# Kernel tuning notes

Hardware: AMD Instinct MI355X
Metric: run time of the kernel (lower is better)

The kernel has to match this reference:

```python
import jax, jax.numpy as jnp
import numpy as np

N = 50000
E = 800000
F_IN, F_HID, F_OUT = 128, 128, 64


def setup_inputs() -> dict:
    key = jax.random.key(0)
    ks = jax.random.split(key, 8)
    x = jax.random.normal(ks[0], (N, F_IN), dtype=jnp.float32)
    attn_edge_index = jax.random.randint(ks[1], (2, E), 0, N, dtype=jnp.int64)
    attn_edge_weight = jax.random.uniform(ks[2], (E,), dtype=jnp.float32)
    # GCNConv params (glorot-ish scale); PyG lin has no bias, conv bias added after aggregation
    W1 = jax.random.normal(ks[3], (F_IN, F_HID), dtype=jnp.float32) * (1.0 / np.sqrt(F_IN))
    b1 = jnp.zeros((F_HID,), dtype=jnp.float32)
    W2 = jax.random.normal(ks[4], (F_HID, F_OUT), dtype=jnp.float32) * (1.0 / np.sqrt(F_HID))
    b2 = jnp.zeros((F_OUT,), dtype=jnp.float32)
    return {"x": x, "attn_edge_index": attn_edge_index, "attn_edge_weight": attn_edge_weight,
            "W1": W1, "b1": b1, "W2": W2, "b2": b2}


def _gcn_norm(edge_index, edge_weight, num_nodes):
    # Add self-loops with weight 1 (PyG gcn_norm default)
    loop = jnp.arange(num_nodes, dtype=edge_index.dtype)
    src = jnp.concatenate([edge_index[0], loop])
    dst = jnp.concatenate([edge_index[1], loop])
    w = jnp.concatenate([edge_weight, jnp.ones((num_nodes,), edge_weight.dtype)])
    deg = jax.ops.segment_sum(w, dst, num_segments=num_nodes)  # in-degree weighted
    dinv = jnp.where(deg > 0, jax.lax.rsqrt(deg), 0.0)
    norm = dinv[src] * w * dinv[dst]  # symmetric normalization
    return src, dst, norm


def _gcn_conv(h, src, dst, norm, W, b, num_nodes):
    h = h @ W                                   # [N, Fout] dense transform
    msg = norm[:, None] * h[src]                # [E+N, Fout] gather-multiply
    out = jax.ops.segment_sum(msg, dst, num_segments=num_nodes)  # scatter-add
    return out + b


def reference(x, attn_edge_index, attn_edge_weight, W1, b1, W2, b2):
    num_nodes = x.shape[0]
    src, dst, norm = _gcn_norm(attn_edge_index, attn_edge_weight, num_nodes)
    h = _gcn_conv(x, src, dst, norm, W1, b1, num_nodes)
    h = jax.nn.relu(h)
    # dropout(p=0.5) is identity in eval mode
    h = _gcn_conv(h, src, dst, norm, W2, b2, num_nodes)
    return h
```

## Files before the change

kernel.cpp:

```cpp
#include <hip/hip_runtime.h>
#include <hip/hip_bf16.h>

static constexpr int FIN   = 128;
static constexpr int FHID  = 128;
static constexpr int FOUTC = 64;
static constexpr int CAP   = 64;

typedef short bf16x8 __attribute__((ext_vector_type(8)));
typedef float f32x4 __attribute__((ext_vector_type(4)));
typedef unsigned u32x2 __attribute__((ext_vector_type(2)));
typedef unsigned u32x4 __attribute__((ext_vector_type(4)));

__device__ __forceinline__ float bfbits2f(unsigned short u) {
  union { unsigned i; float f; } c; c.i = ((unsigned)u) << 16; return c.f;
}
__device__ __forceinline__ float wbits2f(unsigned u) {
  union { unsigned i; float f; } c; c.i = u; return c.f;
}
__device__ __forceinline__ unsigned f2wbits(float f) {
  union { float fv; unsigned i; } c; c.fv = f; return c.i;
}
__device__ __forceinline__ void unpack_bf2(unsigned u, float& lo, float& hi) {
  union { unsigned i; float f; } a, b;
  a.i = u << 16;
  b.i = u & 0xffff0000u;
  lo = a.f; hi = b.f;
}
__device__ __forceinline__ unsigned short f2bfbits(float f) {
  union { float fv; unsigned i; } c; c.fv = f;
  unsigned i = c.i;
  unsigned r = i + 0x7FFFu + ((i >> 16) & 1u);
  if ((i & 0x7F800000u) == 0x7F800000u) r = i;
  return (unsigned short)(r >> 16);
}
__device__ __forceinline__ int ld_idx(const void* ei, int is64, long long off) {
  return is64 ? (int)((const long long*)ei)[off] : ((const int*)ei)[off];
}
__device__ __forceinline__ float ld_f(const void* p, int isbf, long long i) {
  return isbf ? bfbits2f(((const unsigned short*)p)[i]) : ((const float*)p)[i];
}

__global__ void setup_kernel(const unsigned short* __restrict__ xb,
                             const unsigned* __restrict__ eiw,
                             const void* __restrict__ W1, const void* __restrict__ W2,
                             int* __restrict__ flags, unsigned short* __restrict__ Wt1,
                             unsigned short* __restrict__ Wt2, uint4* __restrict__ ellz,
                             int nell4) {
  const int tid = threadIdx.x;
  const int gid = blockIdx.x * 256 + tid;
  __shared__ int sflags[2];
  if (tid < 64) {
    unsigned short xs = xb[2 * tid];
    unsigned long long mb = __ballot(((xs >> 7) & 0xFFu) >= 0xC0u);
    unsigned long long m2 = __ballot(eiw[2 * tid + 1] != 0u);
    if (tid == 0) {
      sflags[0] = (mb == 0ull);
      sflags[1] = (m2 == 0ull);
      if (blockIdx.x == 0) { flags[0] = sflags[0]; flags[1] = sflags[1]; }
    }
  }
  __syncthreads();
  int f = sflags[0];
  if (blockIdx.x < 96) {
    int i = gid;
    if (i < 128 * 128) {
      int k = i >> 7, nn = i & 127;
      Wt1[nn * 128 + k] = f2bfbits(ld_f(W1, f, i));
    } else {
      int j = i - 128 * 128;
      int k = j >> 6, nn = j & 63;
      Wt2[nn * 128 + k] = f2bfbits(ld_f(W2, f, j));
    }
  }
  uint4 z = make_uint4(0u, 0u, 0u, 0u);
  for (int j = gid; j < nell4; j += gridDim.x * 256) ellz[j] = z;
}

__global__ void fill_ell(const void* __restrict__ ei, const void* __restrict__ ew,
                         const int* __restrict__ flg, unsigned long long* __restrict__ ell,
                         int E, int half) {
  int g = blockIdx.x * 256 + threadIdx.x;
  if (g >= half) return;
  int is64 = flg[1], isbf = flg[0];
  int sA = ld_idx(ei, is64, g);
  int dA = ld_idx(ei, is64, (long long)E + g);
  unsigned wA = f2wbits(ld_f(ew, isbf, g));
  int eB = g + half;
  bool hasB = eB < E;
  int sB = 0, dB = 0;
  unsigned wB = 0u;
  if (hasB) {
    sB = ld_idx(ei, is64, eB);
    dB = ld_idx(ei, is64, (long long)E + eB);
    wB = f2wbits(ld_f(ew, isbf, eB));
  }
  unsigned long long vA = ((unsigned long long)wA << 32) | (unsigned)sA;
  unsigned long long vB = ((unsigned long long)wB << 32) | (unsigned)sB;
  unsigned long long* rowA = ell + (size_t)dA * CAP;
  unsigned long long* rowB = ell + (size_t)dB * CAP;
  int pA = g & (CAP - 1), pB = eB & (CAP - 1);
  bool doneA = (vA == 0ull);
  bool doneB = !hasB || (vB == 0ull);
  unsigned long long oA = doneA ? 0ull : atomicCAS(&rowA[pA], 0ull, vA);
  unsigned long long oB = doneB ? 0ull : atomicCAS(&rowB[pB], 0ull, vB);
  for (int t = 1; t < CAP && !doneA && oA != 0ull; ++t) {
    pA = (pA + 1) & (CAP - 1);
    oA = atomicCAS(&rowA[pA], 0ull, vA);
  }
  for (int t = 1; t < CAP && !doneB && oB != 0ull; ++t) {
    pB = (pB + 1) & (CAP - 1);
    oB = atomicCAS(&rowB[pB], 0ull, vB);
  }
}

__global__ void dinv_compact(uint2* __restrict__ ell, float* __restrict__ dinv,
                             unsigned* __restrict__ cedge, int n) {
  int wid = (blockIdx.x * 256 + threadIdx.x) >> 6;
  int lane = threadIdx.x & 63;
  if (wid >= n) return;
  u32x2 rv = __builtin_nontemporal_load((const u32x2*)(ell + (size_t)wid * CAP) + lane);
  float w = wbits2f(rv.y);
  float ws = w;
#pragma unroll
  for (int off = 1; off < 64; off <<= 1) ws += __shfl_xor(ws, off);
  bool valid = rv.y != 0u;
  unsigned long long m = __ballot(valid);
  int c = __popcll(m);
  int rank = __popcll(m & ((1ull << lane) - 1ull));
  int destl = valid ? rank : c + (lane - rank);
  unsigned entry = valid ? ((rv.x << 16) | (unsigned)f2bfbits(w)) : 0u;
  int pe = __builtin_amdgcn_ds_permute(destl << 2, (int)entry);
  cedge[(size_t)wid * (CAP * 2) + lane] = (unsigned)pe;
  if (lane == 0) dinv[wid] = rsqrtf(1.f + ws);
}

__launch_bounds__(256)
__global__ void gather_l1(const void* __restrict__ x, const int* __restrict__ flg,
                          const unsigned* __restrict__ cedge, const float* __restrict__ dinv,
                          unsigned* __restrict__ agg, int n) {
  int wid = (blockIdx.x * 256 + threadIdx.x) >> 6;
  int lane = threadIdx.x & 63;
  if (wid >= n) return;
  unsigned e = __builtin_nontemporal_load(cedge + (size_t)wid * (CAP * 2) + lane);
  unsigned long long m = __ballot(e != 0u);
  int c = __popcll(m);
  int rsrc = (int)(e >> 16);
  float rw = (lane < c) ? bfbits2f((unsigned short)(e & 0xFFFFu)) * dinv[rsrc] : 0.f;
  float di = dinv[wid];

  if (flg[0]) {
    const uint4* xv = (const uint4*)x;
    const int fgrp = lane & 15, egrp = lane >> 4;
    float acc[8];
#pragma unroll
    for (int k = 0; k < 8; ++k) acc[k] = 0.f;
    int iters = (c + 15) >> 4;
    for (int it = 0; it < iters; ++it) {
      int b = it * 16 + egrp;
      int i0 = b, i1 = b + 4, i2 = b + 8, i3 = b + 12;
      int s0 = __shfl(rsrc, i0), s1 = __shfl(rsrc, i1);
      int s2 = __shfl(rsrc, i2), s3 = __shfl(rsrc, i3);
      float w0 = __shfl(rw, i0), w1 = __shfl(rw, i1);
      float w2 = __shfl(rw, i2), w3 = __shfl(rw, i3);
      s0 = i0 < c ? s0 : wid;
      s1 = i1 < c ? s1 : wid;
      s2 = i2 < c ? s2 : wid;
      s3 = i3 < c ? s3 : wid;
      uint4 u0 = xv[(size_t)s0 * 16 + fgrp];
      uint4 u1 = xv[(size_t)s1 * 16 + fgrp];
      uint4 u2 = xv[(size_t)s2 * 16 + fgrp];
      uint4 u3 = xv[(size_t)s3 * 16 + fgrp];
      float l, h;
      unpack_bf2(u0.x, l, h); acc[0] = fmaf(w0, l, acc[0]); acc[1] = fmaf(w0, h, acc[1]);
      unpack_bf2(u0.y, l, h); acc[2] = fmaf(w0, l, acc[2]); acc[3] = fmaf(w0, h, acc[3]);
      unpack_bf2(u0.z, l, h); acc[4] = fmaf(w0, l, acc[4]); acc[5] = fmaf(w0, h, acc[5]);
      unpack_bf2(u0.w, l, h); acc[6] = fmaf(w0, l, acc[6]); acc[7] = fmaf(w0, h, acc[7]);
      unpack_bf2(u1.x, l, h); acc[0] = fmaf(w1, l, acc[0]); acc[1] = fmaf(w1, h, acc[1]);
      unpack_bf2(u1.y, l, h); acc[2] = fmaf(w1, l, acc[2]); acc[3] = fmaf(w1, h, acc[3]);
      unpack_bf2(u1.z, l, h); acc[4] = fmaf(w1, l, acc[4]); acc[5] = fmaf(w1, h, acc[5]);
      unpack_bf2(u1.w, l, h); acc[6] = fmaf(w1, l, acc[6]); acc[7] = fmaf(w1, h, acc[7]);
      unpack_bf2(u2.x, l, h); acc[0] = fmaf(w2, l, acc[0]); acc[1] = fmaf(w2, h, acc[1]);
      unpack_bf2(u2.y, l, h); acc[2] = fmaf(w2, l, acc[2]); acc[3] = fmaf(w2, h, acc[3]);
      unpack_bf2(u2.z, l, h); acc[4] = fmaf(w2, l, acc[4]); acc[5] = fmaf(w2, h, acc[5]);
      unpack_bf2(u2.w, l, h); acc[6] = fmaf(w2, l, acc[6]); acc[7] = fmaf(w2, h, acc[7]);
      unpack_bf2(u3.x, l, h); acc[0] = fmaf(w3, l, acc[0]); acc[1] = fmaf(w3, h, acc[1]);
      unpack_bf2(u3.y, l, h); acc[2] = fmaf(w3, l, acc[2]); acc[3] = fmaf(w3, h, acc[3]);
      unpack_bf2(u3.z, l, h); acc[4] = fmaf(w3, l, acc[4]); acc[5] = fmaf(w3, h, acc[5]);
      unpack_bf2(u3.w, l, h); acc[6] = fmaf(w3, l, acc[6]); acc[7] = fmaf(w3, h, acc[7]);
    }
#pragma unroll
    for (int k = 0; k < 8; ++k) {
      acc[k] += __shfl_xor(acc[k], 16);
      acc[k] += __shfl_xor(acc[k], 32);
    }
    if (lane < 16) {
      uint4 su = xv[(size_t)wid * 16 + fgrp];
      float s0, s1, s2, s3, s4, s5, s6, s7;
      unpack_bf2(su.x, s0, s1); unpack_bf2(su.y, s2, s3);
      unpack_bf2(su.z, s4, s5); unpack_bf2(su.w, s6, s7);
      float dd = di * di;
      float o0 = di * acc[0] + dd * s0, o1 = di * acc[1] + dd * s1;
      float o2 = di * acc[2] + dd * s2, o3 = di * acc[3] + dd * s3;
      float o4 = di * acc[4] + dd * s4, o5 = di * acc[5] + dd * s5;
      float o6 = di * acc[6] + dd * s6, o7 = di * acc[7] + dd * s7;
      u32x4 pk;
      pk.x = (unsigned)f2bfbits(o0) | ((unsigned)f2bfbits(o1) << 16);
      pk.y = (unsigned)f2bfbits(o2) | ((unsigned)f2bfbits(o3) << 16);
      pk.z = (unsigned)f2bfbits(o4) | ((unsigned)f2bfbits(o5) << 16);
      pk.w = (unsigned)f2bfbits(o6) | ((unsigned)f2bfbits(o7) << 16);
      __builtin_nontemporal_store(pk, (u32x4*)agg + (size_t)wid * 16 + fgrp);
    }
  } else {
    const float4* xf = (const float4*)x;
    const int fgrp = lane & 31, egrp = lane >> 5;
    float acc[4] = {0.f, 0.f, 0.f, 0.f};
    int it8 = (c + 7) >> 3;
    for (int it = 0; it < it8; ++it) {
      int b = it * 8 + egrp;
#pragma unroll
      for (int t = 0; t < 4; ++t) {
        int idx = b + t * 2;
        int s = __shfl(rsrc, idx);
        float w = __shfl(rw, idx);
        s = idx < c ? s : wid;
        float4 v = xf[(size_t)s * 32 + fgrp];
        acc[0] = fmaf(w, v.x, acc[0]); acc[1] = fmaf(w, v.y, acc[1]);
        acc[2] = fmaf(w, v.z, acc[2]); acc[3] = fmaf(w, v.w, acc[3]);
      }
    }
#pragma unroll
    for (int k = 0; k < 4; ++k) acc[k] += __shfl_xor(acc[k], 32);
    if (lane < 32) {
      float4 sv = xf[(size_t)wid * 32 + fgrp];
      float dd = di * di;
      float o0 = di * acc[0] + dd * sv.x, o1 = di * acc[1] + dd * sv.y;
      float o2 = di * acc[2] + dd * sv.z, o3 = di * acc[3] + dd * sv.w;
      uint2 pk;
      pk.x = (unsigned)f2bfbits(o0) | ((unsigned)f2bfbits(o1) << 16);
      pk.y = (unsigned)f2bfbits(o2) | ((unsigned)f2bfbits(o3) << 16);
      ((uint2*)agg)[(size_t)wid * 32 + fgrp] = pk;
    }
  }
}

__launch_bounds__(256)
__global__ void gather_l2(const unsigned short* __restrict__ hw2, const int* __restrict__ flg,
                          const unsigned* __restrict__ cedge, const float* __restrict__ dinv,
                          const void* __restrict__ b2, void* __restrict__ out, int n) {
  int wid = (blockIdx.x * 256 + threadIdx.x) >> 6;
  int lane = threadIdx.x & 63;
  if (wid >= n) return;
  unsigned e = __builtin_nontemporal_load(cedge + (size_t)wid * (CAP * 2) + lane);
  unsigned long long m = __ballot(e != 0u);
  int c = __popcll(m);
  int rsrc = (int)(e >> 16);
  float rw = (lane < c) ? bfbits2f((unsigned short)(e & 0xFFFFu)) * dinv[rsrc] : 0.f;
  float di = dinv[wid];

  const uint4* hv = (const uint4*)hw2;
  const int fgrp = lane & 7, egrp = lane >> 3;
  float acc[8];
#pragma unroll
  for (int k = 0; k < 8; ++k) acc[k] = 0.f;
  int iters = (c + 15) >> 4;
  for (int it = 0; it < iters; ++it) {
    int i0 = it * 16 + egrp, i1 = i0 + 8;
    int s0 = __shfl(rsrc, i0), s1 = __shfl(rsrc, i1);
    float w0 = __shfl(rw, i0), w1 = __shfl(rw, i1);
    s0 = i0 < c ? s0 : wid;
    s1 = i1 < c ? s1 : wid;
    uint4 u0 = hv[(size_t)s0 * 8 + fgrp];
    uint4 u1 = hv[(size_t)s1 * 8 + fgrp];
    float l, h;
    unpack_bf2(u0.x, l, h); acc[0] = fmaf(w0, l, acc[0]); acc[1] = fmaf(w0, h, acc[1]);
    unpack_bf2(u0.y, l, h); acc[2] = fmaf(w0, l, acc[2]); acc[3] = fmaf(w0, h, acc[3]);
    unpack_bf2(u0.z, l, h); acc[4] = fmaf(w0, l, acc[4]); acc[5] = fmaf(w0, h, acc[5]);
    unpack_bf2(u0.w, l, h); acc[6] = fmaf(w0, l, acc[6]); acc[7] = fmaf(w0, h, acc[7]);
    unpack_bf2(u1.x, l, h); acc[0] = fmaf(w1, l, acc[0]); acc[1] = fmaf(w1, h, acc[1]);
    unpack_bf2(u1.y, l, h); acc[2] = fmaf(w1, l, acc[2]); acc[3] = fmaf(w1, h, acc[3]);
    unpack_bf2(u1.z, l, h); acc[4] = fmaf(w1, l, acc[4]); acc[5] = fmaf(w1, h, acc[5]);
    unpack_bf2(u1.w, l, h); acc[6] = fmaf(w1, l, acc[6]); acc[7] = fmaf(w1, h, acc[7]);
  }
#pragma unroll
  for (int k = 0; k < 8; ++k) {
    acc[k] += __shfl_xor(acc[k], 8);
    acc[k] += __shfl_xor(acc[k], 16);
    acc[k] += __shfl_xor(acc[k], 32);
  }
  if (lane < 8) {
    int isbf = flg[0];
    uint4 su = hv[(size_t)wid * 8 + fgrp];
    float s0, s1, s2, s3, s4, s5, s6, s7;
    unpack_bf2(su.x, s0, s1); unpack_bf2(su.y, s2, s3);
    unpack_bf2(su.z, s4, s5); unpack_bf2(su.w, s6, s7);
    float dd = di * di;
    float o0 = di * acc[0] + dd * s0 + ld_f(b2, isbf, fgrp * 8 + 0);
    float o1 = di * acc[1] + dd * s1 + ld_f(b2, isbf, fgrp * 8 + 1);
    float o2 = di * acc[2] + dd * s2 + ld_f(b2, isbf, fgrp * 8 + 2);
    float o3 = di * acc[3] + dd * s3 + ld_f(b2, isbf, fgrp * 8 + 3);
    float o4 = di * acc[4] + dd * s4 + ld_f(b2, isbf, fgrp * 8 + 4);
    float o5 = di * acc[5] + dd * s5 + ld_f(b2, isbf, fgrp * 8 + 5);
    float o6 = di * acc[6] + dd * s6 + ld_f(b2, isbf, fgrp * 8 + 6);
    float o7 = di * acc[7] + dd * s7 + ld_f(b2, isbf, fgrp * 8 + 7);
    if (isbf) {
      uint4 pk;
      pk.x = (unsigned)f2bfbits(o0) | ((unsigned)f2bfbits(o1) << 16);
      pk.y = (unsigned)f2bfbits(o2) | ((unsigned)f2bfbits(o3) << 16);
      pk.z = (unsigned)f2bfbits(o4) | ((unsigned)f2bfbits(o5) << 16);
      pk.w = (unsigned)f2bfbits(o6) | ((unsigned)f2bfbits(o7) << 16);
      ((uint4*)out)[(size_t)wid * 8 + fgrp] = pk;
    } else {
      ((float4*)out)[(size_t)wid * 16 + fgrp * 2 + 0] = make_float4(o0, o1, o2, o3);
      ((float4*)out)[(size_t)wid * 16 + fgrp * 2 + 1] = make_float4(o4, o5, o6, o7);
    }
  }
}

__launch_bounds__(256)
__global__ void gemm12(const unsigned short* __restrict__ agg1,
                       const unsigned short* __restrict__ Wt1,
                       const unsigned short* __restrict__ Wt2,
                       const void* __restrict__ b1, const int* __restrict__ flg,
                       unsigned short* __restrict__ hw2, int M) {
  __shared__ unsigned short As[128 * 128];
  __shared__ unsigned short W1s[128 * 128];
  __shared__ unsigned short W2s[64 * 128];
  const int tid = threadIdx.x;
  const int r0 = blockIdx.x * 128;

  for (int i = tid; i < 128 * 16; i += 256) {
    int r = i >> 4, ch = i & 15;
    uint4 v = make_uint4(0u, 0u, 0u, 0u);
    if (r0 + r < M) v = *(const uint4*)(agg1 + (size_t)(r0 + r) * 128 + ch * 8);
    *(uint4*)&As[r * 128 + ((ch ^ (r & 15)) << 3)] = v;
  }
  for (int i = tid; i < 128 * 16; i += 256) {
    int r = i >> 4, ch = i & 15;
    uint4 v = *(const uint4*)(Wt1 + (size_t)r * 128 + ch * 8);
    *(uint4*)&W1s[r * 128 + ((ch ^ (r & 15)) << 3)] = v;
  }
  for (int i = tid; i < 64 * 16; i += 256) {
    int r = i >> 4, ch = i & 15;
    uint4 v = *(const uint4*)(Wt2 + (size_t)r * 128 + ch * 8);
    *(uint4*)&W2s[r * 128 + ((ch ^ (r & 15)) << 3)] = v;
  }
  __syncthreads();

  const int lane = tid & 63;
  const int wv = tid >> 6;
  const int ln15 = lane & 15;
  const int kq = lane >> 4;
  const int wbf = flg[0];

  f32x4 acc1[2][8];
#pragma unroll
  for (int mi = 0; mi < 2; ++mi)
#pragma unroll
    for (int nt = 0; nt < 8; ++nt) acc1[mi][nt] = (f32x4){0.f, 0.f, 0.f, 0.f};
#pragma unroll
  for (int kc = 0; kc < 4; ++kc) {
    int coff = (((kc * 4 + kq) ^ ln15) << 3);
    bf16x8 a0 = *(const bf16x8*)&As[((2 * wv + 0) * 16 + ln15) * 128 + coff];
    bf16x8 a1 = *(const bf16x8*)&As[((2 * wv + 1) * 16 + ln15) * 128 + coff];
#pragma unroll
    for (int nt = 0; nt < 8; ++nt) {
      bf16x8 b = *(const bf16x8*)&W1s[(nt * 16 + ln15) * 128 + coff];
      acc1[0][nt] = __builtin_amdgcn_mfma_f32_16x16x32_bf16(a0, b, acc1[0][nt], 0, 0, 0);
      acc1[1][nt] = __builtin_amdgcn_mfma_f32_16x16x32_bf16(a1, b, acc1[1][nt], 0, 0, 0);
    }
  }

#pragma unroll
  for (int nt = 0; nt < 8; ++nt) {
    int col = nt * 16 + ln15;
    float bv = ld_f(b1, wbf, col);
#pragma unroll
    for (int mi = 0; mi < 2; ++mi) {
#pragma unroll
      for (int r = 0; r < 4; ++r) {
        int row = 32 * wv + mi * 16 + kq * 4 + r;
        float o = fmaxf(acc1[mi][nt][r] + bv, 0.f);
        As[row * 128 + ((((col >> 3)) ^ (row & 15)) << 3) + (col & 7)] = f2bfbits(o);
      }
    }
  }
  __syncthreads();

  f32x4 acc2[2][4];
#pragma unroll
  for (int mi = 0; mi < 2; ++mi)
#pragma unroll
    for (int nt = 0; nt < 4; ++nt) acc2[mi][nt] = (f32x4){0.f, 0.f, 0.f, 0.f};
#pragma unroll
  for (int kc = 0; kc < 4; ++kc) {
    int coff = (((kc * 4 + kq) ^ ln15) << 3);
    bf16x8 a0 = *(const bf16x8*)&As[((2 * wv + 0) * 16 + ln15) * 128 + coff];
    bf16x8 a1 = *(const bf16x8*)&As[((2 * wv + 1) * 16 + ln15) * 128 + coff];
#pragma unroll
    for (int nt = 0; nt < 4; ++nt) {
      bf16x8 b = *(const bf16x8*)&W2s[(nt * 16 + ln15) * 128 + coff];
      acc2[0][nt] = __builtin_amdgcn_mfma_f32_16x16x32_bf16(a0, b, acc2[0][nt], 0, 0, 0);
      acc2[1][nt] = __builtin_amdgcn_mfma_f32_16x16x32_bf16(a1, b, acc2[1][nt], 0, 0, 0);
    }
  }
#pragma unroll
  for (int nt = 0; nt < 4; ++nt) {
    int col = nt * 16 + ln15;
#pragma unroll
    for (int mi = 0; mi < 2; ++mi) {
#pragma unroll
      for (int r = 0; r < 4; ++r) {
        int gr = r0 + 32 * wv + mi * 16 + kq * 4 + r;
        if (gr < M) hw2[(size_t)gr * 64 + col] = f2bfbits(acc2[mi][nt][r]);
      }
    }
  }
}

extern "C" void kernel_launch(void* const* d_in, const int* in_sizes, int n_in, void* d_out,
                              int out_size, void* d_ws, size_t ws_size, hipStream_t stream) {
  const void* x  = d_in[0];
  const void* ei = d_in[1];
  const void* ew = d_in[2];
  const void* W1 = d_in[3];
  const void* b1 = d_in[4];
  const void* W2 = d_in[5];
  const void* b2 = d_in[6];

  const int N = in_sizes[0] / FIN;
  const int E = in_sizes[1] / 2;
  const int B = 256;

  int* flags   = (int*)d_ws;
  float* dinv  = (float*)(flags + 16);
  unsigned short* Wt1 = (unsigned short*)(dinv + N);
  unsigned short* Wt2 = Wt1 + 128 * 128;
  unsigned long long* ell = (unsigned long long*)(Wt2 + 64 * 128);
  unsigned* cedge = (unsigned*)ell;
  unsigned short* agg1 = (unsigned short*)(ell + (size_t)N * CAP);
  unsigned short* hw2  = agg1 + (size_t)N * FHID;

  const int half = (E + 1) / 2;
  setup_kernel<<<512, B, 0, stream>>>((const unsigned short*)x, (const unsigned*)ei, W1, W2,
                                      flags, Wt1, Wt2, (uint4*)ell, N * CAP / 2);
  fill_ell<<<(half + B - 1) / B, B, 0, stream>>>(ei, ew, flags, ell, E, half);
  dinv_compact<<<(N + 3) / 4, B, 0, stream>>>((uint2*)ell, dinv, cedge, N);
  gather_l1<<<(N + 3) / 4, B, 0, stream>>>(x, flags, cedge, dinv, (unsigned*)agg1, N);
  gemm12<<<(N + 127) / 128, B, 0, stream>>>(agg1, Wt1, Wt2, b1, flags, hw2, N);
  gather_l2<<<(N + 3) / 4, B, 0, stream>>>(hw2, flags, cedge, dinv, b2, d_out, N);
}
```

Before: 232.1 us.

## Replace CAS hash-ELL build with atomic counter bucketing and fold self-loop into gather

Drops the 64-bit ELL table and its CAS linear probing, along with the separate dinv_compact pass. Edges are now bucketed with a per-destination atomic counter, and degree is accumulated with float atomics. The self-loop is handled as an extra slot in the gather, and the gathers are software-pipelined with double-buffered loads. This removes zeroing a large ELL array, a whole kernel launch and CAS contention, at the cost of nondeterministic edge order, float atomic sums and recomputing rsqrt per neighbor.

```diff
diff --git a/kernel.cpp b/kernel.cpp
--- a/kernel.cpp
+++ b/kernel.cpp
@@ -8,17 +8,10 @@
 
 typedef short bf16x8 __attribute__((ext_vector_type(8)));
 typedef float f32x4 __attribute__((ext_vector_type(4)));
-typedef unsigned u32x2 __attribute__((ext_vector_type(2)));
 typedef unsigned u32x4 __attribute__((ext_vector_type(4)));
 
 __device__ __forceinline__ float bfbits2f(unsigned short u) {
   union { unsigned i; float f; } c; c.i = ((unsigned)u) << 16; return c.f;
-}
-__device__ __forceinline__ float wbits2f(unsigned u) {
-  union { unsigned i; float f; } c; c.i = u; return c.f;
-}
-__device__ __forceinline__ unsigned f2wbits(float f) {
-  union { float fv; unsigned i; } c; c.fv = f; return c.i;
 }
 __device__ __forceinline__ void unpack_bf2(unsigned u, float& lo, float& hi) {
   union { unsigned i; float f; } a, b;
@@ -44,8 +37,8 @@
                              const unsigned* __restrict__ eiw,
                              const void* __restrict__ W1, const void* __restrict__ W2,
                              int* __restrict__ flags, unsigned short* __restrict__ Wt1,
-                             unsigned short* __restrict__ Wt2, uint4* __restrict__ ellz,
-                             int nell4) {
+                             unsigned short* __restrict__ Wt2, uint4* __restrict__ zr,
+                             int nz4, int nztot) {
   const int tid = threadIdx.x;
   const int gid = blockIdx.x * 256 + tid;
   __shared__ int sflags[2];
@@ -73,80 +66,45 @@
     }
   }
   uint4 z = make_uint4(0u, 0u, 0u, 0u);
-  for (int j = gid; j < nell4; j += gridDim.x * 256) ellz[j] = z;
-}
-
-__global__ void fill_ell(const void* __restrict__ ei, const void* __restrict__ ew,
-                         const int* __restrict__ flg, unsigned long long* __restrict__ ell,
-                         int E, int half) {
+  for (int j = gid; j < nz4; j += gridDim.x * 256) zr[j] = z;
+  if (gid == 0) {
+    for (int j = nz4 * 4; j < nztot; ++j) ((unsigned*)zr)[j] = 0u;
+  }
+}
+
+__global__ void fill_edges(const void* __restrict__ ei, const void* __restrict__ ew,
+                           const int* __restrict__ flg, unsigned* __restrict__ cnt,
+                           float* __restrict__ deg, unsigned* __restrict__ cedge, int E) {
   int g = blockIdx.x * 256 + threadIdx.x;
-  if (g >= half) return;
+  if (g >= E) return;
   int is64 = flg[1], isbf = flg[0];
-  int sA = ld_idx(ei, is64, g);
-  int dA = ld_idx(ei, is64, (long long)E + g);
-  unsigned wA = f2wbits(ld_f(ew, isbf, g));
-  int eB = g + half;
-  bool hasB = eB < E;
-  int sB = 0, dB = 0;
-  unsigned wB = 0u;
-  if (hasB) {
-    sB = ld_idx(ei, is64, eB);
-    dB = ld_idx(ei, is64, (long long)E + eB);
-    wB = f2wbits(ld_f(ew, isbf, eB));
-  }
-  unsigned long long vA = ((unsigned long long)wA << 32) | (unsigned)sA;
-  unsigned long long vB = ((unsigned long long)wB << 32) | (unsigned)sB;
-  unsigned long long* rowA = ell + (size_t)dA * CAP;
-  unsigned long long* rowB = ell + (size_t)dB * CAP;
-  int pA = g & (CAP - 1), pB = eB & (CAP - 1);
-  bool doneA = (vA == 0ull);
-  bool doneB = !hasB || (vB == 0ull);
-  unsigned long long oA = doneA ? 0ull : atomicCAS(&rowA[pA], 0ull, vA);
-  unsigned long long oB = doneB ? 0ull : atomicCAS(&rowB[pB], 0ull, vB);
-  for (int t = 1; t < CAP && !doneA && oA != 0ull; ++t) {
-    pA = (pA + 1) & (CAP - 1);
-    oA = atomicCAS(&rowA[pA], 0ull, vA);
-  }
-  for (int t = 1; t < CAP && !doneB && oB != 0ull; ++t) {
-    pB = (pB + 1) & (CAP - 1);
-    oB = atomicCAS(&rowB[pB], 0ull, vB);
-  }
-}
-
-__global__ void dinv_compact(uint2* __restrict__ ell, float* __restrict__ dinv,
-                             unsigned* __restrict__ cedge, int n) {
+  int s = ld_idx(ei, is64, g);
+  int d = ld_idx(ei, is64, (long long)E + g);
+  float w = ld_f(ew, isbf, g);
+  unsigned pos = atomicAdd(&cnt[d], 1u);
+  atomicAdd(&deg[d], w);
+  if (pos < (unsigned)CAP)
+    cedge[(size_t)d * CAP + pos] = (((unsigned)s) << 16) | (unsigned)f2bfbits(w);
+}
+
+__launch_bounds__(256)
+__global__ void gather_l1(const void* __restrict__ x, const int* __restrict__ flg,
+                          const unsigned* __restrict__ cedge, const unsigned* __restrict__ cnt,
+                          const float* __restrict__ deg, unsigned* __restrict__ agg, int n) {
   int wid = (blockIdx.x * 256 + threadIdx.x) >> 6;
   int lane = threadIdx.x & 63;
   if (wid >= n) return;
-  u32x2 rv = __builtin_nontemporal_load((const u32x2*)(ell + (size_t)wid * CAP) + lane);
-  float w = wbits2f(rv.y);
-  float ws = w;
-#pragma unroll
-  for (int off = 1; off < 64; off <<= 1) ws += __shfl_xor(ws, off);
-  bool valid = rv.y != 0u;
-  unsigned long long m = __ballot(valid);
-  int c = __popcll(m);
-  int rank = __popcll(m & ((1ull << lane) - 1ull));
-  int destl = valid ? rank : c + (lane - rank);
-  unsigned entry = valid ? ((rv.x << 16) | (unsigned)f2bfbits(w)) : 0u;
-  int pe = __builtin_amdgcn_ds_permute(destl << 2, (int)entry);
-  cedge[(size_t)wid * (CAP * 2) + lane] = (unsigned)pe;
-  if (lane == 0) dinv[wid] = rsqrtf(1.f + ws);
-}
-
-__launch_bounds__(256)
-__global__ void gather_l1(const void* __restrict__ x, const int* __restrict__ flg,
-                          const unsigned* __restrict__ cedge, const float* __restrict__ dinv,
-                          unsigned* __restrict__ agg, int n) {
-  int wid = (blockIdx.x * 256 + threadIdx.x) >> 6;
-  int lane = threadIdx.x & 63;
-  if (wid >= n) return;
-  unsigned e = __builtin_nontemporal_load(cedge + (size_t)wid * (CAP * 2) + lane);
-  unsigned long long m = __ballot(e != 0u);
-  int c = __popcll(m);
-  int rsrc = (int)(e >> 16);
-  float rw = (lane < c) ? bfbits2f((unsigned short)(e & 0xFFFFu)) * dinv[rsrc] : 0.f;
-  float di = dinv[wid];
+  unsigned e = __builtin_nontemporal_load(cedge + (size_t)wid * CAP + lane);
+  int c = (int)cnt[wid];
+  c = c > CAP ? CAP : c;
+  float dw = deg[wid];
+  float di = rsqrtf(1.f + dw);
+  int rs = (lane < c) ? (int)(e >> 16) : wid;
+  float ds = deg[rs];
+  float wv = (lane < c) ? bfbits2f((unsigned short)(e & 0xFFFFu)) : 1.f;
+  int cp = c + 1; if (cp > 64) cp = 64;
+  float rw = (lane < cp) ? wv * rsqrtf(1.f + ds) : 0.f;
+  int iters = (cp + 15) >> 4;
 
   if (flg[0]) {
     const uint4* xv = (const uint4*)x;
@@ -154,55 +112,62 @@
     float acc[8];
 #pragma unroll
     for (int k = 0; k < 8; ++k) acc[k] = 0.f;
-    int iters = (c + 15) >> 4;
-    for (int it = 0; it < iters; ++it) {
-      int b = it * 16 + egrp;
-      int i0 = b, i1 = b + 4, i2 = b + 8, i3 = b + 12;
-      int s0 = __shfl(rsrc, i0), s1 = __shfl(rsrc, i1);
-      int s2 = __shfl(rsrc, i2), s3 = __shfl(rsrc, i3);
-      float w0 = __shfl(rw, i0), w1 = __shfl(rw, i1);
-      float w2 = __shfl(rw, i2), w3 = __shfl(rw, i3);
-      s0 = i0 < c ? s0 : wid;
-      s1 = i1 < c ? s1 : wid;
-      s2 = i2 < c ? s2 : wid;
-      s3 = i3 < c ? s3 : wid;
-      uint4 u0 = xv[(size_t)s0 * 16 + fgrp];
-      uint4 u1 = xv[(size_t)s1 * 16 + fgrp];
-      uint4 u2 = xv[(size_t)s2 * 16 + fgrp];
-      uint4 u3 = xv[(size_t)s3 * 16 + fgrp];
-      float l, h;
-      unpack_bf2(u0.x, l, h); acc[0] = fmaf(w0, l, acc[0]); acc[1] = fmaf(w0, h, acc[1]);
-      unpack_bf2(u0.y, l, h); acc[2] = fmaf(w0, l, acc[2]); acc[3] = fmaf(w0, h, acc[3]);
-      unpack_bf2(u0.z, l, h); acc[4] = fmaf(w0, l, acc[4]); acc[5] = fmaf(w0, h, acc[5]);
-      unpack_bf2(u0.w, l, h); acc[6] = fmaf(w0, l, acc[6]); acc[7] = fmaf(w0, h, acc[7]);
-      unpack_bf2(u1.x, l, h); acc[0] = fmaf(w1, l, acc[0]); acc[1] = fmaf(w1, h, acc[1]);
-      unpack_bf2(u1.y, l, h); acc[2] = fmaf(w1, l, acc[2]); acc[3] = fmaf(w1, h, acc[3]);
-      unpack_bf2(u1.z, l, h); acc[4] = fmaf(w1, l, acc[4]); acc[5] = fmaf(w1, h, acc[5]);
-      unpack_bf2(u1.w, l, h); acc[6] = fmaf(w1, l, acc[6]); acc[7] = fmaf(w1, h, acc[7]);
-      unpack_bf2(u2.x, l, h); acc[0] = fmaf(w2, l, acc[0]); acc[1] = fmaf(w2, h, acc[1]);
-      unpack_bf2(u2.y, l, h); acc[2] = fmaf(w2, l, acc[2]); acc[3] = fmaf(w2, h, acc[3]);
-      unpack_bf2(u2.z, l, h); acc[4] = fmaf(w2, l, acc[4]); acc[5] = fmaf(w2, h, acc[5]);
-      unpack_bf2(u2.w, l, h); acc[6] = fmaf(w2, l, acc[6]); acc[7] = fmaf(w2, h, acc[7]);
-      unpack_bf2(u3.x, l, h); acc[0] = fmaf(w3, l, acc[0]); acc[1] = fmaf(w3, h, acc[1]);
-      unpack_bf2(u3.y, l, h); acc[2] = fmaf(w3, l, acc[2]); acc[3] = fmaf(w3, h, acc[3]);
-      unpack_bf2(u3.z, l, h); acc[4] = fmaf(w3, l, acc[4]); acc[5] = fmaf(w3, h, acc[5]);
-      unpack_bf2(u3.w, l, h); acc[6] = fmaf(w3, l, acc[6]); acc[7] = fmaf(w3, h, acc[7]);
-    }
+
+#define L1_LOAD(UA, UB, UC, UD, WA, WB, WC, WD, base)                       \
+    {                                                                       \
+      int i0 = (base) + egrp, i1 = i0 + 4, i2 = i0 + 8, i3 = i0 + 12;       \
+      int s0 = __shfl(rs, i0), s1 = __shfl(rs, i1);                         \
+      int s2 = __shfl(rs, i2), s3 = __shfl(rs, i3);                         \
+      UA = xv[(size_t)s0 * 16 + fgrp];                                      \
+      UB = xv[(size_t)s1 * 16 + fgrp];                                      \
+      UC = xv[(size_t)s2 * 16 + fgrp];                                      \
+      UD = xv[(size_t)s3 * 16 + fgrp];                                      \
+      WA = __shfl(rw, i0); WB = __shfl(rw, i1);                             \
+      WC = __shfl(rw, i2); WD = __shfl(rw, i3);                             \
+    }
+#define L1_FMA(U, W)                                                        \
+    { float l, h;                                                           \
+      unpack_bf2(U.x, l, h); acc[0]=fmaf(W,l,acc[0]); acc[1]=fmaf(W,h,acc[1]); \
+      unpack_bf2(U.y, l, h); acc[2]=fmaf(W,l,acc[2]); acc[3]=fmaf(W,h,acc[3]); \
+      unpack_bf2(U.z, l, h); acc[4]=fmaf(W,l,acc[4]); acc[5]=fmaf(W,h,acc[5]); \
+      unpack_bf2(U.w, l, h); acc[6]=fmaf(W,l,acc[6]); acc[7]=fmaf(W,h,acc[7]); }
+#define L1_FMA4(UA,UB,UC,UD,WA,WB,WC,WD) \
+    L1_FMA(UA,WA) L1_FMA(UB,WB) L1_FMA(UC,WC) L1_FMA(UD,WD)
+
+    uint4 a0, a1, a2, a3, b0, b1, b2, b3;
+    float wa0, wa1, wa2, wa3, wb0, wb1, wb2, wb3;
+    L1_LOAD(a0, a1, a2, a3, wa0, wa1, wa2, wa3, 0);
+    if (iters > 1) {
+      L1_LOAD(b0, b1, b2, b3, wb0, wb1, wb2, wb3, 16);
+      L1_FMA4(a0, a1, a2, a3, wa0, wa1, wa2, wa3);
+      if (iters > 2) {
+        L1_LOAD(a0, a1, a2, a3, wa0, wa1, wa2, wa3, 32);
+        L1_FMA4(b0, b1, b2, b3, wb0, wb1, wb2, wb3);
+        if (iters > 3) {
+          L1_LOAD(b0, b1, b2, b3, wb0, wb1, wb2, wb3, 48);
+          L1_FMA4(a0, a1, a2, a3, wa0, wa1, wa2, wa3);
+          L1_FMA4(b0, b1, b2, b3, wb0, wb1, wb2, wb3);
+        } else {
+          L1_FMA4(a0, a1, a2, a3, wa0, wa1, wa2, wa3);
+        }
+      } else {
+        L1_FMA4(b0, b1, b2, b3, wb0, wb1, wb2, wb3);
+      }
+    } else {
+      L1_FMA4(a0, a1, a2, a3, wa0, wa1, wa2, wa3);
+    }
+#undef L1_LOAD
+#undef L1_FMA
+#undef L1_FMA4
+
 #pragma unroll
     for (int k = 0; k < 8; ++k) {
       acc[k] += __shfl_xor(acc[k], 16);
       acc[k] += __shfl_xor(acc[k], 32);
     }
     if (lane < 16) {
-      uint4 su = xv[(size_t)wid * 16 + fgrp];
-      float s0, s1, s2, s3, s4, s5, s6, s7;
-      unpack_bf2(su.x, s0, s1); unpack_bf2(su.y, s2, s3);
-      unpack_bf2(su.z, s4, s5); unpack_bf2(su.w, s6, s7);
-      float dd = di * di;
-      float o0 = di * acc[0] + dd * s0, o1 = di * acc[1] + dd * s1;
-      float o2 = di * acc[2] + dd * s2, o3 = di * acc[3] + dd * s3;
-      float o4 = di * acc[4] + dd * s4, o5 = di * acc[5] + dd * s5;
-      float o6 = di * acc[6] + dd * s6, o7 = di * acc[7] + dd * s7;
+      float o0 = di * acc[0], o1 = di * acc[1], o2 = di * acc[2], o3 = di * acc[3];
+      float o4 = di * acc[4], o5 = di * acc[5], o6 = di * acc[6], o7 = di * acc[7];
       u32x4 pk;
       pk.x = (unsigned)f2bfbits(o0) | ((unsigned)f2bfbits(o1) << 16);
       pk.y = (unsigned)f2bfbits(o2) | ((unsigned)f2bfbits(o3) << 16);
@@ -214,15 +179,14 @@
     const float4* xf = (const float4*)x;
     const int fgrp = lane & 31, egrp = lane >> 5;
     float acc[4] = {0.f, 0.f, 0.f, 0.f};
-    int it8 = (c + 7) >> 3;
+    int it8 = (cp + 7) >> 3;
     for (int it = 0; it < it8; ++it) {
       int b = it * 8 + egrp;
 #pragma unroll
       for (int t = 0; t < 4; ++t) {
         int idx = b + t * 2;
-        int s = __shfl(rsrc, idx);
+        int s = __shfl(rs, idx);
         float w = __shfl(rw, idx);
-        s = idx < c ? s : wid;
         float4 v = xf[(size_t)s * 32 + fgrp];
         acc[0] = fmaf(w, v.x, acc[0]); acc[1] = fmaf(w, v.y, acc[1]);
         acc[2] = fmaf(w, v.z, acc[2]); acc[3] = fmaf(w, v.w, acc[3]);
@@ -231,10 +195,7 @@
 #pragma unroll
     for (int k = 0; k < 4; ++k) acc[k] += __shfl_xor(acc[k], 32);
     if (lane < 32) {
-      float4 sv = xf[(size_t)wid * 32 + fgrp];
-      float dd = di * di;
-      float o0 = di * acc[0] + dd * sv.x, o1 = di * acc[1] + dd * sv.y;
-      float o2 = di * acc[2] + dd * sv.z, o3 = di * acc[3] + dd * sv.w;
+      float o0 = di * acc[0], o1 = di * acc[1], o2 = di * acc[2], o3 = di * acc[3];
       uint2 pk;
       pk.x = (unsigned)f2bfbits(o0) | ((unsigned)f2bfbits(o1) << 16);
       pk.y = (unsigned)f2bfbits(o2) | ((unsigned)f2bfbits(o3) << 16);
@@ -245,42 +206,70 @@
 
 __launch_bounds__(256)
 __global__ void gather_l2(const unsigned short* __restrict__ hw2, const int* __restrict__ flg,
-                          const unsigned* __restrict__ cedge, const float* __restrict__ dinv,
-                          const void* __restrict__ b2, void* __restrict__ out, int n) {
+                          const unsigned* __restrict__ cedge, const unsigned* __restrict__ cnt,
+                          const float* __restrict__ deg, const void* __restrict__ b2,
+                          void* __restrict__ out, int n) {
   int wid = (blockIdx.x * 256 + threadIdx.x) >> 6;
   int lane = threadIdx.x & 63;
   if (wid >= n) return;
-  unsigned e = __builtin_nontemporal_load(cedge + (size_t)wid * (CAP * 2) + lane);
-  unsigned long long m = __ballot(e != 0u);
-  int c = __popcll(m);
-  int rsrc = (int)(e >> 16);
-  float rw = (lane < c) ? bfbits2f((unsigned short)(e & 0xFFFFu)) * dinv[rsrc] : 0.f;
-  float di = dinv[wid];
+  unsigned e = __builtin_nontemporal_load(cedge + (size_t)wid * CAP + lane);
+  int c = (int)cnt[wid];
+  c = c > CAP ? CAP : c;
+  float dw = deg[wid];
+  float di = rsqrtf(1.f + dw);
+  int rs = (lane < c) ? (int)(e >> 16) : wid;
+  float ds = deg[rs];
+  float wv = (lane < c) ? bfbits2f((unsigned short)(e & 0xFFFFu)) : 1.f;
+  int cp = c + 1; if (cp > 64) cp = 64;
+  float rw = (lane < cp) ? wv * rsqrtf(1.f + ds) : 0.f;
+  int iters = (cp + 15) >> 4;
 
   const uint4* hv = (const uint4*)hw2;
   const int fgrp = lane & 7, egrp = lane >> 3;
   float acc[8];
 #pragma unroll
   for (int k = 0; k < 8; ++k) acc[k] = 0.f;
-  int iters = (c + 15) >> 4;
-  for (int it = 0; it < iters; ++it) {
-    int i0 = it * 16 + egrp, i1 = i0 + 8;
-    int s0 = __shfl(rsrc, i0), s1 = __shfl(rsrc, i1);
-    float w0 = __shfl(rw, i0), w1 = __shfl(rw, i1);
-    s0 = i0 < c ? s0 : wid;
-    s1 = i1 < c ? s1 : wid;
-    uint4 u0 = hv[(size_t)s0 * 8 + fgrp];
-    uint4 u1 = hv[(size_t)s1 * 8 + fgrp];
-    float l, h;
-    unpack_bf2(u0.x, l, h); acc[0] = fmaf(w0, l, acc[0]); acc[1] = fmaf(w0, h, acc[1]);
-    unpack_bf2(u0.y, l, h); acc[2] = fmaf(w0, l, acc[2]); acc[3] = fmaf(w0, h, acc[3]);
-    unpack_bf2(u0.z, l, h); acc[4] = fmaf(w0, l, acc[4]); acc[5] = fmaf(w0, h, acc[5]);
-    unpack_bf2(u0.w, l, h); acc[6] = fmaf(w0, l, acc[6]); acc[7] = fmaf(w0, h, acc[7]);
-    unpack_bf2(u1.x, l, h); acc[0] = fmaf(w1, l, acc[0]); acc[1] = fmaf(w1, h, acc[1]);
-    unpack_bf2(u1.y, l, h); acc[2] = fmaf(w1, l, acc[2]); acc[3] = fmaf(w1, h, acc[3]);
-    unpack_bf2(u1.z, l, h); acc[4] = fmaf(w1, l, acc[4]); acc[5] = fmaf(w1, h, acc[5]);
-    unpack_bf2(u1.w, l, h); acc[6] = fmaf(w1, l, acc[6]); acc[7] = fmaf(w1, h, acc[7]);
-  }
+
+#define L2_LOAD(UA, UB, WA, WB, base)                                   \
+  { int i0 = (base) + egrp, i1 = i0 + 8;                                \
+    int s0 = __shfl(rs, i0), s1 = __shfl(rs, i1);                       \
+    UA = hv[(size_t)s0 * 8 + fgrp];                                     \
+    UB = hv[(size_t)s1 * 8 + fgrp];                                     \
+    WA = __shfl(rw, i0); WB = __shfl(rw, i1); }
+#define L2_FMA(U, W)                                                    \
+  { float l, h;                                                         \
+    unpack_bf2(U.x, l, h); acc[0]=fmaf(W,l,acc[0]); acc[1]=fmaf(W,h,acc[1]); \
+    unpack_bf2(U.y, l, h); acc[2]=fmaf(W,l,acc[2]); acc[3]=fmaf(W,h,acc[3]); \
+    unpack_bf2(U.z, l, h); acc[4]=fmaf(W,l,acc[4]); acc[5]=fmaf(W,h,acc[5]); \
+    unpack_bf2(U.w, l, h); acc[6]=fmaf(W,l,acc[6]); acc[7]=fmaf(W,h,acc[7]); }
+#define L2_FMA2(UA, UB, WA, WB) L2_FMA(UA, WA) L2_FMA(UB, WB)
+
+  uint4 a0, a1, b0, b1;
+  float wa0, wa1, wb0, wb1;
+  L2_LOAD(a0, a1, wa0, wa1, 0);
+  if (iters > 1) {
+    L2_LOAD(b0, b1, wb0, wb1, 16);
+    L2_FMA2(a0, a1, wa0, wa1);
+    if (iters > 2) {
+      L2_LOAD(a0, a1, wa0, wa1, 32);
+      L2_FMA2(b0, b1, wb0, wb1);
+      if (iters > 3) {
+        L2_LOAD(b0, b1, wb0, wb1, 48);
+        L2_FMA2(a0, a1, wa0, wa1);
+        L2_FMA2(b0, b1, wb0, wb1);
+      } else {
+        L2_FMA2(a0, a1, wa0, wa1);
+      }
+    } else {
+      L2_FMA2(b0, b1, wb0, wb1);
+    }
+  } else {
+    L2_FMA2(a0, a1, wa0, wa1);
+  }
+#undef L2_LOAD
+#undef L2_FMA
+#undef L2_FMA2
+
 #pragma unroll
   for (int k = 0; k < 8; ++k) {
     acc[k] += __shfl_xor(acc[k], 8);
@@ -289,19 +278,14 @@
   }
   if (lane < 8) {
     int isbf = flg[0];
-    uint4 su = hv[(size_t)wid * 8 + fgrp];
-    float s0, s1, s2, s3, s4, s5, s6, s7;
-    unpack_bf2(su.x, s0, s1); unpack_bf2(su.y, s2, s3);
-    unpack_bf2(su.z, s4, s5); unpack_bf2(su.w, s6, s7);
-    float dd = di * di;
-    float o0 = di * acc[0] + dd * s0 + ld_f(b2, isbf, fgrp * 8 + 0);
-    float o1 = di * acc[1] + dd * s1 + ld_f(b2, isbf, fgrp * 8 + 1);
-    float o2 = di * acc[2] + dd * s2 + ld_f(b2, isbf, fgrp * 8 + 2);
-    float o3 = di * acc[3] + dd * s3 + ld_f(b2, isbf, fgrp * 8 + 3);
-    float o4 = di * acc[4] + dd * s4 + ld_f(b2, isbf, fgrp * 8 + 4);
-    float o5 = di * acc[5] + dd * s5 + ld_f(b2, isbf, fgrp * 8 + 5);
-    float o6 = di * acc[6] + dd * s6 + ld_f(b2, isbf, fgrp * 8 + 6);
-    float o7 = di * acc[7] + dd * s7 + ld_f(b2, isbf, fgrp * 8 + 7);
+    float o0 = di * acc[0] + ld_f(b2, isbf, fgrp * 8 + 0);
+    float o1 = di * acc[1] + ld_f(b2, isbf, fgrp * 8 + 1);
+    float o2 = di * acc[2] + ld_f(b2, isbf, fgrp * 8 + 2);
+    float o3 = di * acc[3] + ld_f(b2, isbf, fgrp * 8 + 3);
+    float o4 = di * acc[4] + ld_f(b2, isbf, fgrp * 8 + 4);
+    float o5 = di * acc[5] + ld_f(b2, isbf, fgrp * 8 + 5);
+    float o6 = di * acc[6] + ld_f(b2, isbf, fgrp * 8 + 6);
+    float o7 = di * acc[7] + ld_f(b2, isbf, fgrp * 8 + 7);
     if (isbf) {
       uint4 pk;
       pk.x = (unsigned)f2bfbits(o0) | ((unsigned)f2bfbits(o1) << 16);
@@ -432,20 +416,21 @@
   const int B = 256;
 
   int* flags   = (int*)d_ws;
-  float* dinv  = (float*)(flags + 16);
-  unsigned short* Wt1 = (unsigned short*)(dinv + N);
+  unsigned* cnt = (unsigned*)(flags + 16);
+  float* deg   = (float*)(cnt + N);
+  unsigned short* Wt1 = (unsigned short*)(deg + N);
   unsigned short* Wt2 = Wt1 + 128 * 128;
-  unsigned long long* ell = (unsigned long long*)(Wt2 + 64 * 128);
-  unsigned* cedge = (unsigned*)ell;
-  unsigned short* agg1 = (unsigned short*)(ell + (size_t)N * CAP);
+  unsigned* cedge = (unsigned*)(Wt2 + 64 * 128);
+  unsigned short* agg1 = (unsigned short*)(cedge + (size_t)N * CAP);
   unsigned short* hw2  = agg1 + (size_t)N * FHID;
 
-  const int half = (E + 1) / 2;
-  setup_kernel<<<512, B, 0, stream>>>((const unsigned short*)x, (const unsigned*)ei, W1, W2,
-                                      flags, Wt1, Wt2, (uint4*)ell, N * CAP / 2);
-  fill_ell<<<(half + B - 1) / B, B, 0, stream>>>(ei, ew, flags, ell, E, half);
-  dinv_compact<<<(N + 3) / 4, B, 0, stream>>>((uint2*)ell, dinv, cedge, N);
-  gather_l1<<<(N + 3) / 4, B, 0, stream>>>(x, flags, cedge, dinv, (unsigned*)agg1, N);
+  const int nztot = 2 * N;
+  const int nz4 = nztot >> 2;
+
+  setup_kernel<<<256, B, 0, stream>>>((const unsigned short*)x, (const unsigned*)ei, W1, W2,
+                                      flags, Wt1, Wt2, (uint4*)cnt, nz4, nztot);
+  fill_edges<<<(E + B - 1) / B, B, 0, stream>>>(ei, ew, flags, cnt, deg, cedge, E);
+  gather_l1<<<(N + 3) / 4, B, 0, stream>>>(x, flags, cedge, cnt, deg, (unsigned*)agg1, N);
   gemm12<<<(N + 127) / 128, B, 0, stream>>>(agg1, Wt1, Wt2, b1, flags, hw2, N);
-  gather_l2<<<(N + 3) / 4, B, 0, stream>>>(hw2, flags, cedge, dinv, b2, d_out, N);
-}
+  gather_l2<<<(N + 3) / 4, B, 0, stream>>>(hw2, flags, cedge, cnt, deg, b2, d_out, N);
+}
```

Result: slower. 262.6 us (+13.2%).
